# Kernel optimization log

Hardware: AMD Instinct MI355X
Metric: run time of the kernel (lower is better)

The kernel has to match this reference:

```python
import math
import jax, jax.numpy as jnp
import numpy as np


def _gelu(x):
    return jax.nn.gelu(x, approximate=False)


def _bilinear_sample(feat, gx, gy):
    """grid_sample, mode=bilinear, padding=border, align_corners=True.
    feat: [B,C,H,W]; gx,gy: [B,M] in [-1,1]. Returns [B,M,C]."""
    B, C, H, W = feat.shape
    x = jnp.clip((gx + 1.0) * 0.5 * (W - 1), 0.0, W - 1)
    y = jnp.clip((gy + 1.0) * 0.5 * (H - 1), 0.0, H - 1)
    x0 = jnp.floor(x); y0 = jnp.floor(y)
    wx = (x - x0)[..., None]; wy = (y - y0)[..., None]
    x0i = x0.astype(jnp.int32); y0i = y0.astype(jnp.int32)
    x1i = jnp.minimum(x0i + 1, W - 1); y1i = jnp.minimum(y0i + 1, H - 1)
    ft = jnp.transpose(feat, (0, 2, 3, 1))  # [B,H,W,C]
    gather = jax.vmap(lambda f, yi, xi: f[yi, xi])
    v00 = gather(ft, y0i, x0i); v01 = gather(ft, y0i, x1i)
    v10 = gather(ft, y1i, x0i); v11 = gather(ft, y1i, x1i)
    return (v00 * (1 - wx) * (1 - wy) + v01 * wx * (1 - wy)
            + v10 * (1 - wx) * wy + v11 * wx * wy)


def _layernorm(x, w, b, eps=1e-5):
    m = jnp.mean(x, -1, keepdims=True)
    v = jnp.var(x, -1, keepdims=True)
    return (x - m) / jnp.sqrt(v + eps) * w + b


def _gfb(h, f_next, ph_w, ph_b, gate, w1, b1, w2, b2, ln_w, ln_b):
    g = jax.nn.sigmoid(gate)
    fused = f_next + g * (h @ ph_w + ph_b)
    fused = _gelu(fused @ w1 + b1) @ w2 + b2
    return _layernorm(fused, ln_w, ln_b)


def _forward(img, feat_s8, feat_s16, coarse_flow, query_coords,
             pp_w1, pp_b1, pp_w2, pp_b2, p8_w, p8_b, p16_w, p16_b,
             f1_ph_w, f1_ph_b, f1_gate, f1_w1, f1_b1, f1_w2, f1_b2, f1_ln_w, f1_ln_b,
             f2_ph_w, f2_ph_b, f2_gate, f2_w1, f2_b1, f2_w2, f2_b2, f2_ln_w, f2_ln_b,
             h_w1, h_b1, h_w2, h_b2, h_w3, h_b3):
    B, _, H, W = img.shape
    N = query_coords.shape[1]
    k = 5; half = k // 2
    H8, W8 = coarse_flow.shape[2], coarse_flow.shape[3]
    # normalized grid at query points (x,y)
    gx = 2.0 * query_coords[..., 0] / (W - 1) - 1.0
    gy = 2.0 * query_coords[..., 1] / (H - 1) - 1.0
    coarse_q = _bilinear_sample(coarse_flow, gx, gy)  # [B,N,2]
    coarse_q = coarse_q * jnp.array([W / W8, H / H8], coarse_q.dtype)
    # local k x k RGB patches
    offs = jnp.arange(-half, half + 1, dtype=img.dtype)
    oy, ox = jnp.meshgrid(offs, offs, indexing='ij')
    og = jnp.stack([ox.reshape(-1), oy.reshape(-1)], -1)  # [k*k,2]
    ce = query_coords[:, :, None, :] + og                # [B,N,kk,2]
    pgx = (2.0 * ce[..., 0] / (W - 1) - 1.0).reshape(B, -1)
    pgy = (2.0 * ce[..., 1] / (H - 1) - 1.0).reshape(B, -1)
    patches = _bilinear_sample(img, pgx, pgy).reshape(B, N, k * k * 3)
    f_local = _gelu(patches @ pp_w1 + pp_b1) @ pp_w2 + pp_b2
    f8 = _bilinear_sample(feat_s8, gx, gy) @ p8_w + p8_b
    f16 = _bilinear_sample(feat_s16, gx, gy) @ p16_w + p16_b
    D = f_local.shape[-1]
    h = f_local.reshape(B * N, D)
    h = _gfb(h, f8.reshape(B * N, D), f1_ph_w, f1_ph_b, f1_gate,
             f1_w1, f1_b1, f1_w2, f1_b2, f1_ln_w, f1_ln_b)
    h = _gfb(h, f16.reshape(B * N, D), f2_ph_w, f2_ph_b, f2_gate,
             f2_w1, f2_b1, f2_w2, f2_b2, f2_ln_w, f2_ln_b)
    # relative-in-cell coords + sinusoidal PE (6 bands)
    qx = query_coords[..., 0] / (W / W8)
    qy = query_coords[..., 1] / (H / H8)
    local = jnp.stack([(qx - jnp.round(qx)) * 2.0, (qy - jnp.round(qy)) * 2.0], -1)
    freqs = (2.0 ** jnp.arange(6, dtype=local.dtype)) * math.pi
    xf = local[..., None] * freqs                        # [B,N,2,6]
    enc = jnp.concatenate([jnp.sin(xf), jnp.cos(xf)], -1).reshape(B, N, 24)
    pe = jnp.concatenate([local, enc], -1).reshape(B * N, 26)
    coarse_flat = coarse_q.reshape(B * N, 2)
    mi = jnp.concatenate([h, pe, coarse_flat], -1)       # [B*N, 156]
    delta = _gelu(_gelu(mi @ h_w1 + h_b1) @ h_w2 + h_b2) @ h_w3 + h_b3
    return (coarse_flat + delta).reshape(B, N, 2)


def setup_inputs() -> dict:
    key = jax.random.key(0)
    ks = jax.random.split(key, 40)
    B, H, W = 2, 384, 512
    H8, W8, H16, W16 = 48, 64, 24, 32
    N, D, k = 65536, 128, 5
    pf = 3 * k * k
    def p(i, shape):
        return jax.random.normal(ks[i], shape, jnp.float32) * 0.05
    return {
        'img': jax.random.uniform(ks[0], (B, 3, H, W), jnp.float32),
        'feat_s8': jax.random.normal(ks[1], (B, D, H8, W8), jnp.float32),
        'feat_s16': jax.random.normal(ks[2], (B, D, H16, W16), jnp.float32),
        'coarse_flow': jax.random.normal(ks[3], (B, 2, H8, W8), jnp.float32),
        'query_coords': jax.random.uniform(ks[4], (B, N, 2), jnp.float32)
                        * jnp.array([W - 1.0, H - 1.0], jnp.float32),
        'pp_w1': p(5, (pf, D)), 'pp_b1': p(6, (D,)),
        'pp_w2': p(7, (D, D)), 'pp_b2': p(8, (D,)),
        'p8_w': p(9, (D, D)), 'p8_b': p(10, (D,)),
        'p16_w': p(11, (D, D)), 'p16_b': p(12, (D,)),
        'f1_ph_w': p(13, (D, D)), 'f1_ph_b': p(14, (D,)), 'f1_gate': p(15, (D,)),
        'f1_w1': p(16, (D, 2 * D)), 'f1_b1': p(17, (2 * D,)),
        'f1_w2': p(18, (2 * D, D)), 'f1_b2': p(19, (D,)),
        'f1_ln_w': 1.0 + p(20, (D,)), 'f1_ln_b': p(21, (D,)),
        'f2_ph_w': p(22, (D, D)), 'f2_ph_b': p(23, (D,)), 'f2_gate': p(24, (D,)),
        'f2_w1': p(25, (D, 2 * D)), 'f2_b1': p(26, (2 * D,)),
        'f2_w2': p(27, (2 * D, D)), 'f2_b2': p(28, (D,)),
        'f2_ln_w': 1.0 + p(29, (D,)), 'f2_ln_b': p(30, (D,)),
        'h_w1': p(31, (D + 26 + 2, 128)), 'h_b1': p(32, (128,)),
        'h_w2': p(33, (128, 64)), 'h_b2': p(34, (64,)),
        'h_w3': p(35, (64, 2)), 'h_b3': p(36, (2,)),
    }


def reference(img, feat_s8, feat_s16, coarse_flow, query_coords,
              pp_w1, pp_b1, pp_w2, pp_b2, p8_w, p8_b, p16_w, p16_b,
              f1_ph_w, f1_ph_b, f1_gate, f1_w1, f1_b1, f1_w2, f1_b2, f1_ln_w, f1_ln_b,
              f2_ph_w, f2_ph_b, f2_gate, f2_w1, f2_b1, f2_w2, f2_b2, f2_ln_w, f2_ln_b,
              h_w1, h_b1, h_w2, h_b2, h_w3, h_b3):
    return _forward(img, feat_s8, feat_s16, coarse_flow, query_coords,
                    pp_w1, pp_b1, pp_w2, pp_b2, p8_w, p8_b, p16_w, p16_b,
                    f1_ph_w, f1_ph_b, f1_gate, f1_w1, f1_b1, f1_w2, f1_b2, f1_ln_w, f1_ln_b,
                    f2_ph_w, f2_ph_b, f2_gate, f2_w1, f2_b1, f2_w2, f2_b2, f2_ln_w, f2_ln_b,
                    h_w1, h_b1, h_w2, h_b2, h_w3, h_b3)
```

## Files before the change

kernel.cpp:

```cpp
#include <hip/hip_runtime.h>
#include <math.h>

#define NT 512
#define MB 32
#define MTOT 131072
#define IMG_H 384
#define IMG_W 512
#define H8 48
#define W8 64
#define H16 24
#define W16 32

#define SAB 136
#define SHB 168

typedef _Float16 half8_t __attribute__((ext_vector_type(8)));
typedef _Float16 half4_t __attribute__((ext_vector_type(4)));
typedef float f32x4_t __attribute__((ext_vector_type(4)));
typedef unsigned short u16;

#define PW_PP1    0
#define PW_PP2    12288
#define PW_P8CAT  28672
#define PW_P16CAT 61440
#define PW_F1W1   94208
#define PW_F1W2   126976
#define PW_F2W1   159744
#define PW_F2W2   192512
#define PW_HW1    225280
#define PW_HW2    245760
#define PW_END    253952
#define FT8_OFF   PW_END
#define FT8_CNT   (2*H8*W8*128)
#define FT16_OFF  (FT8_OFF + FT8_CNT)
#define FT16_CNT  (2*H16*W16*128)
#define FB_OFF    (FT16_OFF + FT16_CNT)

__device__ __forceinline__ u16 tohalf(float v) {
  return __builtin_bit_cast(u16, (_Float16)v);
}
__device__ __forceinline__ float geluf(float x) {
  float x2 = x * x;
  float t = x * fmaf(x2, 0.0713548162726f, 1.5957691216057308f);
  float e = __expf(-t);
  return x * __builtin_amdgcn_rcpf(1.0f + e);
}

__device__ __forceinline__ float bilin_plane(const float* __restrict__ plane,
                                             int Wd, int Hd, float x, float y) {
  x = fminf(fmaxf(x, 0.f), (float)(Wd - 1));
  y = fminf(fmaxf(y, 0.f), (float)(Hd - 1));
  float x0f = floorf(x), y0f = floorf(y);
  int x0 = (int)x0f, y0 = (int)y0f;
  int x1 = min(x0 + 1, Wd - 1), y1 = min(y0 + 1, Hd - 1);
  float wx = x - x0f, wy = y - y0f;
  const float* r0 = plane + y0 * Wd;
  const float* r1 = plane + y1 * Wd;
  float v00 = r0[x0], v01 = r0[x1], v10 = r1[x0], v11 = r1[x1];
  float top = v00 + wx * (v01 - v00);
  float bot = v10 + wx * (v11 - v10);
  return top + wy * (bot - top);
}

__device__ __forceinline__ void featSample(const u16* __restrict__ ft, int Wd, int Hd,
                                           float x, float y, u16* dstRow, int i16) {
  x = fminf(fmaxf(x, 0.f), (float)(Wd - 1));
  y = fminf(fmaxf(y, 0.f), (float)(Hd - 1));
  float x0f = floorf(x), y0f = floorf(y);
  int x0 = (int)x0f, y0 = (int)y0f;
  int x1 = min(x0 + 1, Wd - 1), y1 = min(y0 + 1, Hd - 1);
  float wx = x - x0f, wy = y - y0f;
  half8_t v00 = *reinterpret_cast<const half8_t*>(ft + (y0 * Wd + x0) * 128 + i16 * 8);
  half8_t v01 = *reinterpret_cast<const half8_t*>(ft + (y0 * Wd + x1) * 128 + i16 * 8);
  half8_t v10 = *reinterpret_cast<const half8_t*>(ft + (y1 * Wd + x0) * 128 + i16 * 8);
  half8_t v11 = *reinterpret_cast<const half8_t*>(ft + (y1 * Wd + x1) * 128 + i16 * 8);
  half8_t r;
#pragma unroll
  for (int j = 0; j < 8; ++j) {
    float top = (float)v00[j] + wx * ((float)v01[j] - (float)v00[j]);
    float bot = (float)v10[j] + wx * ((float)v11[j] - (float)v10[j]);
    r[j] = (_Float16)(top + wy * (bot - top));
  }
  *reinterpret_cast<half8_t*>(dstRow + i16 * 8) = r;
}

template <int NTW, int KT, int SPLITKT, int ACT, int NWAVES = 8>
__device__ __forceinline__ void mmv(
    const u16* __restrict__ wpk,
    const u16* aA, int strA, const u16* aB, int strB,
    const float* __restrict__ bias,
    u16* oA, int ostrA, u16* oB, int ostrB, int oSplitNt) {
  const int tid = threadIdx.x;
  const int lane = tid & 63;
  const int w = tid >> 6;
  const int l15 = lane & 15;
  const int g = lane >> 4;
  if (NWAVES == 8 || w < NWAVES) {
    f32x4_t acc[NTW][2];
#pragma unroll
    for (int i = 0; i < NTW; ++i) {
      acc[i][0] = (f32x4_t){0.f, 0.f, 0.f, 0.f};
      acc[i][1] = (f32x4_t){0.f, 0.f, 0.f, 0.f};
    }
#pragma unroll
    for (int kt = 0; kt < KT; ++kt) {
      const u16* ab = (kt < SPLITKT) ? (aA + kt * 32) : (aB + (kt - SPLITKT) * 32);
      const int str = (kt < SPLITKT) ? strA : strB;
      half8_t af0 = *reinterpret_cast<const half8_t*>(ab + l15 * str + g * 8);
      half8_t af1 = *reinterpret_cast<const half8_t*>(ab + (16 + l15) * str + g * 8);
#pragma unroll
      for (int i = 0; i < NTW; ++i) {
        const int nt = w + (i << 3);
        half8_t bf = *reinterpret_cast<const half8_t*>(wpk + ((nt * KT + kt) * 64 + lane) * 8);
        acc[i][0] = __builtin_amdgcn_mfma_f32_16x16x32_f16(bf, af0, acc[i][0], 0, 0, 0);
        acc[i][1] = __builtin_amdgcn_mfma_f32_16x16x32_f16(bf, af1, acc[i][1], 0, 0, 0);
      }
    }
#pragma unroll
    for (int i = 0; i < NTW; ++i) {
      const int nt = w + (i << 3);
      const int colg = nt << 4;
      f32x4_t bv = *reinterpret_cast<const f32x4_t*>(bias + colg + (g << 2));
      u16* ob; int colB, ostr;
      if (nt < oSplitNt) { ob = oA; colB = colg; ostr = ostrA; }
      else { ob = oB; colB = colg - (oSplitNt << 4); ostr = ostrB; }
#pragma unroll
      for (int mt = 0; mt < 2; ++mt) {
        const int row = (mt << 4) + l15;
        half4_t hv;
#pragma unroll
        for (int r = 0; r < 4; ++r) {
          float v = acc[i][mt][r] + bv[r];
          if (ACT == 1) v = geluf(v);
          hv[r] = (_Float16)v;
        }
        *reinterpret_cast<half4_t*>(ob + row * ostr + colB + (g << 2)) = hv;
      }
    }
  }
}

__device__ __forceinline__ void lnorm(const u16* src, u16* dst,
                                      const float* __restrict__ lw,
                                      const float* __restrict__ lb) {
  const int tid = threadIdx.x;
  int q = tid >> 4, s = tid & 15;
  half8_t v = *reinterpret_cast<const half8_t*>(src + q * SAB + s * 8);
  float xs[8];
  float sum = 0.f, sum2 = 0.f;
#pragma unroll
  for (int j = 0; j < 8; ++j) {
    float x = (float)v[j];
    xs[j] = x; sum += x; sum2 += x * x;
  }
  sum += __shfl_xor(sum, 1); sum2 += __shfl_xor(sum2, 1);
  sum += __shfl_xor(sum, 2); sum2 += __shfl_xor(sum2, 2);
  sum += __shfl_xor(sum, 4); sum2 += __shfl_xor(sum2, 4);
  sum += __shfl_xor(sum, 8); sum2 += __shfl_xor(sum2, 8);
  float mean = sum * 0.0078125f;
  float var = sum2 * 0.0078125f - mean * mean;
  float rstd = rsqrtf(var + 1e-5f);
  half8_t r;
#pragma unroll
  for (int j = 0; j < 8; ++j) {
    int c = s * 8 + j;
    r[j] = (_Float16)((xs[j] - mean) * rstd * lw[c] + lb[c]);
  }
  *reinterpret_cast<half8_t*>(dst + q * SHB + s * 8) = r;
}

struct PackArgs {
  const float *pp_w1, *pp_w2, *p8_w, *f1_ph_w, *f1_gate, *p16_w, *f2_ph_w, *f2_gate;
  const float *f1_w1, *f1_w2, *f2_w1, *f2_w2, *h_w1, *h_w2;
  u16* dst;
};

__global__ void pack_weights(PackArgs a) {
  const int KTs[10]   = {3, 4, 8, 8, 4, 8, 4, 8, 5, 4};
  const int Ks[10]    = {75, 128, 256, 256, 128, 256, 128, 256, 156, 128};
  const int bases[11] = {0, 12288, 28672, 61440, 94208, 126976,
                         159744, 192512, 225280, 245760, 253952};
  int stride = gridDim.x * blockDim.x;
  for (int i = blockIdx.x * blockDim.x + threadIdx.x; i < PW_END; i += stride) {
    int s = 0;
    while (i >= bases[s + 1]) ++s;
    int rem = i - bases[s];
    int e = rem & 511, lane = e >> 3, j = e & 7;
    int ntkt = rem >> 9;
    int kt = ntkt % KTs[s], nt = ntkt / KTs[s];
    int k = kt * 32 + ((lane >> 4) << 3) + j;
    int col = (nt << 4) + (lane & 15);
    float v = 0.f;
    if (k < Ks[s]) {
      switch (s) {
        case 0: v = a.pp_w1[k * 128 + col]; break;
        case 1: v = a.pp_w2[k * 128 + col]; break;
        case 2: v = (k < 128) ? a.p8_w[k * 128 + col]
                              : a.f1_ph_w[(k - 128) * 128 + col] /
                                    (1.f + expf(-a.f1_gate[col])); break;
        case 3: v = (k < 128) ? a.p16_w[k * 128 + col]
                              : a.f2_ph_w[(k - 128) * 128 + col] /
                                    (1.f + expf(-a.f2_gate[col])); break;
        case 4: v = a.f1_w1[k * 256 + col]; break;
        case 5: v = a.f1_w2[k * 128 + col]; break;
        case 6: v = a.f2_w1[k * 256 + col]; break;
        case 7: v = a.f2_w2[k * 128 + col]; break;
        case 8: v = a.h_w1[k * 128 + col]; break;
        case 9: v = a.h_w2[k * 64 + col]; break;
      }
    }
    a.dst[i] = tohalf(v);
  }
}

__global__ void fuse_bias(const float* __restrict__ p8_b, const float* __restrict__ f1_ph_b,
                          const float* __restrict__ f1_gate,
                          const float* __restrict__ p16_b, const float* __restrict__ f2_ph_b,
                          const float* __restrict__ f2_gate, float* __restrict__ fb) {
  int t = threadIdx.x;
  if (t < 128) {
    fb[t] = p8_b[t] + f1_ph_b[t] / (1.f + expf(-f1_gate[t]));
    fb[128 + t] = p16_b[t] + f2_ph_b[t] / (1.f + expf(-f2_gate[t]));
  }
}

__global__ void cvt_cl_f16(const float* __restrict__ src, u16* __restrict__ dst,
                           int Hd, int Wd) {
  int total = 2 * 128 * Hd * Wd;
  int stride = gridDim.x * blockDim.x;
  for (int i = blockIdx.x * blockDim.x + threadIdx.x; i < total; i += stride) {
    int x = i % Wd;
    int t = i / Wd;
    int y = t % Hd; t /= Hd;
    int c = t % 128;
    int b = t / 128;
    dst[((b * Hd + y) * Wd + x) * 128 + c] = tohalf(src[i]);
  }
}

struct KParams {
  const float *img, *coarse_flow, *qc;
  const u16 *wpk, *ft8, *ft16;
  const float *fb;
  const float *pp_b1, *pp_b2;
  const float *f1_b1, *f1_b2, *f1_ln_w, *f1_ln_b;
  const float *f2_b1, *f2_b2, *f2_ln_w, *f2_ln_b;
  const float *h_b1, *h_b2, *h_w3, *h_b3;
  float* out;
};

__global__ __launch_bounds__(NT, 2) void ifd_mfma(KParams P) {
  __shared__ __align__(16) u16 smem[2 * (MB * SAB) + MB * SHB];
  __shared__ float qcL[64];
  __shared__ float cb[64];
  u16* ab0 = smem;
  u16* ab1 = smem + MB * SAB;
  u16* hb  = smem + 2 * MB * SAB;

  const int tid = threadIdx.x;
  const int m0 = blockIdx.x * MB;

  if (tid < 64) qcL[tid] = P.qc[m0 * 2 + tid];
  __syncthreads();

  for (int i = tid; i < MB * 96; i += NT) {
    int q = i / 96, c = i - q * 96;
    u16 val = 0;
    if (c < 75) {
      int m = m0 + q, b = m >> 16;
      float qx = qcL[2 * q], qy = qcL[2 * q + 1];
      int p = c / 3, ch = c - p * 3;
      int iy = p / 5, ix = p - iy * 5;
      const float* plane = P.img + (b * 3 + ch) * (IMG_H * IMG_W);
      val = tohalf(bilin_plane(plane, IMG_W, IMG_H,
                               qx + (float)(ix - 2), qy + (float)(iy - 2)));
    }
    ab0[q * SAB + c] = val;
  }
  for (int i = tid; i < MB * 40; i += NT) {
    int q = i / 40, c = i - q * 40;
    int m = m0 + q, b = m >> 16;
    float qx = qcL[2 * q], qy = qcL[2 * q + 1];
    float val = 0.f;
    if (c < 26) {
      float qx8 = qx * 0.125f, qy8 = qy * 0.125f;
      float lx = (qx8 - rintf(qx8)) * 2.f, ly = (qy8 - rintf(qy8)) * 2.f;
      if (c < 2) val = c ? ly : lx;
      else {
        int k = c - 2;
        int dim = k / 12, tt = k - dim * 12;
        int band = tt % 6, iscos = tt / 6;
        float loc = dim ? ly : lx;
        float ang = loc * 3.14159265358979323846f * (float)(1 << band);
        val = iscos ? __cosf(ang) : __sinf(ang);
      }
    } else if (c < 28) {
      int o = c - 26;
      float x8 = qx * (63.f / 511.f), y8 = qy * (47.f / 383.f);
      float cv = 8.f * bilin_plane(P.coarse_flow + (b * 2 + o) * (H8 * W8), W8, H8, x8, y8);
      cb[q * 2 + o] = cv;
      val = cv;
    }
    hb[q * SHB + 128 + c] = tohalf(val);
  }
  __syncthreads();

  mmv<1, 3, 3, 1>(P.wpk + PW_PP1, ab0, SAB, ab0, SAB, P.pp_b1,
                  ab1, SAB, ab1, SAB, 16);
  __syncthreads();
  mmv<1, 4, 4, 0>(P.wpk + PW_PP2, ab1, SAB, ab1, SAB, P.pp_b2,
                  hb, SHB, hb, SHB, 16);
  for (int i = tid; i < MB * 16; i += NT) {
    int q = i >> 4, i16 = i & 15;
    int m = m0 + q, b = m >> 16;
    float x = qcL[2 * q] * (63.f / 511.f), y = qcL[2 * q + 1] * (47.f / 383.f);
    featSample(P.ft8 + b * (H8 * W8 * 128), W8, H8, x, y, ab0 + q * SAB, i16);
  }
  __syncthreads();
  mmv<1, 8, 4, 0>(P.wpk + PW_P8CAT, ab0, SAB, hb, SHB, P.fb,
                  ab1, SAB, ab1, SAB, 16);
  __syncthreads();
  mmv<2, 4, 4, 1>(P.wpk + PW_F1W1, ab1, SAB, ab1, SAB, P.f1_b1,
                  ab0, SAB, hb, SHB, 8);
  __syncthreads();
  mmv<1, 8, 4, 0>(P.wpk + PW_F1W2, ab0, SAB, hb, SHB, P.f1_b2,
                  ab1, SAB, ab1, SAB, 16);
  __syncthreads();
  lnorm(ab1, hb, P.f1_ln_w, P.f1_ln_b);
  for (int i = tid; i < MB * 16; i += NT) {
    int q = i >> 4, i16 = i & 15;
    int m = m0 + q, b = m >> 16;
    float x = qcL[2 * q] * (31.f / 511.f), y = qcL[2 * q + 1] * (23.f / 383.f);
    featSample(P.ft16 + b * (H16 * W16 * 128), W16, H16, x, y, ab0 + q * SAB, i16);
  }
  __syncthreads();
  mmv<1, 8, 4, 0>(P.wpk + PW_P16CAT, ab0, SAB, hb, SHB, P.fb + 128,
                  ab1, SAB, ab1, SAB, 16);
  __syncthreads();
  mmv<2, 4, 4, 1>(P.wpk + PW_F2W1, ab1, SAB, ab1, SAB, P.f2_b1,
                  ab0, SAB, hb, SHB, 8);
  __syncthreads();
  mmv<1, 8, 4, 0>(P.wpk + PW_F2W2, ab0, SAB, hb, SHB, P.f2_b2,
                  ab1, SAB, ab1, SAB, 16);
  __syncthreads();
  lnorm(ab1, hb, P.f2_ln_w, P.f2_ln_b);
  __syncthreads();
  mmv<1, 5, 5, 1>(P.wpk + PW_HW1, hb, SHB, hb, SHB, P.h_b1,
                  ab1, SAB, ab1, SAB, 16);
  __syncthreads();
  mmv<1, 4, 4, 1, 4>(P.wpk + PW_HW2, ab1, SAB, ab1, SAB, P.h_b2,
                     ab0, SAB, ab0, SAB, 16);
  __syncthreads();
  if (tid < 64) {
    int q = tid >> 1, o = tid & 1;
    float acc = P.h_b3[o];
    const u16* rp = ab0 + q * SAB;
#pragma unroll
    for (int c8 = 0; c8 < 8; ++c8) {
      half8_t v = *reinterpret_cast<const half8_t*>(rp + c8 * 8);
#pragma unroll
      for (int j = 0; j < 8; ++j) acc += (float)v[j] * P.h_w3[(c8 * 8 + j) * 2 + o];
    }
    P.out[(m0 + q) * 2 + o] = cb[q * 2 + o] + acc;
  }
}

extern "C" void kernel_launch(void* const* d_in, const int* in_sizes, int n_in,
                              void* d_out, int out_size, void* d_ws, size_t ws_size,
                              hipStream_t stream) {
  u16* wp = (u16*)d_ws;
  float* fb = (float*)(wp + FB_OFF);

  PackArgs pa;
  pa.pp_w1  = (const float*)d_in[5];
  pa.pp_w2  = (const float*)d_in[7];
  pa.p8_w   = (const float*)d_in[9];
  pa.p16_w  = (const float*)d_in[11];
  pa.f1_ph_w = (const float*)d_in[13];
  pa.f1_gate = (const float*)d_in[15];
  pa.f1_w1  = (const float*)d_in[16];
  pa.f1_w2  = (const float*)d_in[18];
  pa.f2_ph_w = (const float*)d_in[22];
  pa.f2_gate = (const float*)d_in[24];
  pa.f2_w1  = (const float*)d_in[25];
  pa.f2_w2  = (const float*)d_in[27];
  pa.h_w1   = (const float*)d_in[31];
  pa.h_w2   = (const float*)d_in[33];
  pa.dst = wp;
  pack_weights<<<512, 256, 0, stream>>>(pa);
  fuse_bias<<<1, 128, 0, stream>>>((const float*)d_in[10], (const float*)d_in[14],
                                   (const float*)d_in[15], (const float*)d_in[12],
                                   (const float*)d_in[23], (const float*)d_in[24], fb);
  cvt_cl_f16<<<1024, 256, 0, stream>>>((const float*)d_in[1], wp + FT8_OFF, H8, W8);
  cvt_cl_f16<<<256, 256, 0, stream>>>((const float*)d_in[2], wp + FT16_OFF, H16, W16);

  KParams P;
  P.img = (const float*)d_in[0];
  P.coarse_flow = (const float*)d_in[3];
  P.qc = (const float*)d_in[4];
  P.wpk = wp; P.ft8 = wp + FT8_OFF; P.ft16 = wp + FT16_OFF;
  P.fb = fb;
  P.pp_b1 = (const float*)d_in[6];  P.pp_b2 = (const float*)d_in[8];
  P.f1_b1 = (const float*)d_in[17]; P.f1_b2 = (const float*)d_in[19];
  P.f1_ln_w = (const float*)d_in[20]; P.f1_ln_b = (const float*)d_in[21];
  P.f2_b1 = (const float*)d_in[26]; P.f2_b2 = (const float*)d_in[28];
  P.f2_ln_w = (const float*)d_in[29]; P.f2_ln_b = (const float*)d_in[30];
  P.h_b1 = (const float*)d_in[32]; P.h_b2 = (const float*)d_in[34];
  P.h_w3 = (const float*)d_in[35]; P.h_b3 = (const float*)d_in[36];
  P.out = (float*)d_out;

  ifd_mfma<<<MTOT / MB, NT, 0, stream>>>(P);
}
```

Measured before the change: 199.9 us.

## Double rows per block to 64 to reuse each weight fragment across four M-tiles

Raises the number of query rows handled per block from 32 to 64. The MFMA helper now loads four A fragments and issues four MFMAs for each B (weight) fragment, which halves global weight traffic per row. LayerNorm is remapped so 8 threads cover a row instead of 16, and the shared buffers are sized from MB. The cost is more LDS and accumulator registers per block, which may lower occupancy, and half as many blocks in the grid.

```diff
diff --git a/kernel.cpp b/kernel.cpp
--- a/kernel.cpp
+++ b/kernel.cpp
@@ -2,7 +2,7 @@
 #include <math.h>
 
 #define NT 512
-#define MB 32
+#define MB 64
 #define MTOT 131072
 #define IMG_H 384
 #define IMG_W 512
@@ -96,24 +96,26 @@
   const int l15 = lane & 15;
   const int g = lane >> 4;
   if (NWAVES == 8 || w < NWAVES) {
-    f32x4_t acc[NTW][2];
-#pragma unroll
-    for (int i = 0; i < NTW; ++i) {
-      acc[i][0] = (f32x4_t){0.f, 0.f, 0.f, 0.f};
-      acc[i][1] = (f32x4_t){0.f, 0.f, 0.f, 0.f};
-    }
+    f32x4_t acc[NTW][4];
+#pragma unroll
+    for (int i = 0; i < NTW; ++i)
+#pragma unroll
+      for (int mt = 0; mt < 4; ++mt) acc[i][mt] = (f32x4_t){0.f, 0.f, 0.f, 0.f};
 #pragma unroll
     for (int kt = 0; kt < KT; ++kt) {
       const u16* ab = (kt < SPLITKT) ? (aA + kt * 32) : (aB + (kt - SPLITKT) * 32);
       const int str = (kt < SPLITKT) ? strA : strB;
-      half8_t af0 = *reinterpret_cast<const half8_t*>(ab + l15 * str + g * 8);
-      half8_t af1 = *reinterpret_cast<const half8_t*>(ab + (16 + l15) * str + g * 8);
+      half8_t af[4];
+#pragma unroll
+      for (int mt = 0; mt < 4; ++mt)
+        af[mt] = *reinterpret_cast<const half8_t*>(ab + (mt * 16 + l15) * str + g * 8);
 #pragma unroll
       for (int i = 0; i < NTW; ++i) {
         const int nt = w + (i << 3);
         half8_t bf = *reinterpret_cast<const half8_t*>(wpk + ((nt * KT + kt) * 64 + lane) * 8);
-        acc[i][0] = __builtin_amdgcn_mfma_f32_16x16x32_f16(bf, af0, acc[i][0], 0, 0, 0);
-        acc[i][1] = __builtin_amdgcn_mfma_f32_16x16x32_f16(bf, af1, acc[i][1], 0, 0, 0);
+#pragma unroll
+        for (int mt = 0; mt < 4; ++mt)
+          acc[i][mt] = __builtin_amdgcn_mfma_f32_16x16x32_f16(bf, af[mt], acc[i][mt], 0, 0, 0);
       }
     }
 #pragma unroll
@@ -125,7 +127,7 @@
       if (nt < oSplitNt) { ob = oA; colB = colg; ostr = ostrA; }
       else { ob = oB; colB = colg - (oSplitNt << 4); ostr = ostrB; }
 #pragma unroll
-      for (int mt = 0; mt < 2; ++mt) {
+      for (int mt = 0; mt < 4; ++mt) {
         const int row = (mt << 4) + l15;
         half4_t hv;
 #pragma unroll
@@ -144,29 +146,36 @@
                                       const float* __restrict__ lw,
                                       const float* __restrict__ lb) {
   const int tid = threadIdx.x;
-  int q = tid >> 4, s = tid & 15;
-  half8_t v = *reinterpret_cast<const half8_t*>(src + q * SAB + s * 8);
-  float xs[8];
+  int q = tid >> 3, s = tid & 7;
+  const u16* rp = src + q * SAB + s * 16;
+  float xs[16];
   float sum = 0.f, sum2 = 0.f;
 #pragma unroll
-  for (int j = 0; j < 8; ++j) {
-    float x = (float)v[j];
-    xs[j] = x; sum += x; sum2 += x * x;
+  for (int c8 = 0; c8 < 2; ++c8) {
+    half8_t v = *reinterpret_cast<const half8_t*>(rp + c8 * 8);
+#pragma unroll
+    for (int j = 0; j < 8; ++j) {
+      float x = (float)v[j];
+      xs[c8 * 8 + j] = x; sum += x; sum2 += x * x;
+    }
   }
   sum += __shfl_xor(sum, 1); sum2 += __shfl_xor(sum2, 1);
   sum += __shfl_xor(sum, 2); sum2 += __shfl_xor(sum2, 2);
   sum += __shfl_xor(sum, 4); sum2 += __shfl_xor(sum2, 4);
-  sum += __shfl_xor(sum, 8); sum2 += __shfl_xor(sum2, 8);
   float mean = sum * 0.0078125f;
   float var = sum2 * 0.0078125f - mean * mean;
   float rstd = rsqrtf(var + 1e-5f);
-  half8_t r;
-#pragma unroll
-  for (int j = 0; j < 8; ++j) {
-    int c = s * 8 + j;
-    r[j] = (_Float16)((xs[j] - mean) * rstd * lw[c] + lb[c]);
-  }
-  *reinterpret_cast<half8_t*>(dst + q * SHB + s * 8) = r;
+  u16* op = dst + q * SHB + s * 16;
+#pragma unroll
+  for (int c8 = 0; c8 < 2; ++c8) {
+    half8_t r;
+#pragma unroll
+    for (int j = 0; j < 8; ++j) {
+      int c = s * 16 + c8 * 8 + j;
+      r[j] = (_Float16)((xs[c8 * 8 + j] - mean) * rstd * lw[c] + lb[c]);
+    }
+    *reinterpret_cast<half8_t*>(op + c8 * 8) = r;
+  }
 }
 
 struct PackArgs {
@@ -251,8 +260,8 @@
 
 __global__ __launch_bounds__(NT, 2) void ifd_mfma(KParams P) {
   __shared__ __align__(16) u16 smem[2 * (MB * SAB) + MB * SHB];
-  __shared__ float qcL[64];
-  __shared__ float cb[64];
+  __shared__ float qcL[2 * MB];
+  __shared__ float cb[2 * MB];
   u16* ab0 = smem;
   u16* ab1 = smem + MB * SAB;
   u16* hb  = smem + 2 * MB * SAB;
@@ -260,7 +269,7 @@
   const int tid = threadIdx.x;
   const int m0 = blockIdx.x * MB;
 
-  if (tid < 64) qcL[tid] = P.qc[m0 * 2 + tid];
+  if (tid < 2 * MB) qcL[tid] = P.qc[m0 * 2 + tid];
   __syncthreads();
 
   for (int i = tid; i < MB * 96; i += NT) {
@@ -351,7 +360,7 @@
   mmv<1, 4, 4, 1, 4>(P.wpk + PW_HW2, ab1, SAB, ab1, SAB, P.h_b2,
                      ab0, SAB, ab0, SAB, 16);
   __syncthreads();
-  if (tid < 64) {
+  if (tid < 2 * MB) {
     int q = tid >> 1, o = tid & 1;
     float acc = P.h_b3[o];
     const u16* rp = ab0 + q * SAB;
```

New measurement: 182.5 us. 1.1x faster.
